# Kernel tuning notes

Hardware: AMD Instinct MI355X
Metric: run time of the kernel (lower is better)

Reference implementation:

```python
import jax, jax.numpy as jnp
import numpy as np

C = 512
GROUPS = 8
EPS = 1e-5


def setup_inputs() -> dict:
    key = jax.random.key(0)
    ks = jax.random.split(key, 7)
    B, H, W = 16, 32, 32
    x = jax.random.normal(ks[0], (B, C, H, W), dtype=jnp.float32)
    gamma = jnp.ones((C,), jnp.float32)
    beta = jnp.zeros((C,), jnp.float32)
    # 1x1 convs stored as [out, in] matrices
    w_qkv = jax.random.normal(ks[1], (3 * C, C), dtype=jnp.float32) * (1.0 / np.sqrt(C))
    b_qkv = jax.random.normal(ks[2], (3 * C,), dtype=jnp.float32) * 0.02
    w_proj = jax.random.normal(ks[3], (C, C), dtype=jnp.float32) * (1.0 / np.sqrt(C))
    b_proj = jax.random.normal(ks[4], (C,), dtype=jnp.float32) * 0.02
    return {"x": x, "gamma": gamma, "beta": beta, "w_qkv": w_qkv,
            "b_qkv": b_qkv, "w_proj": w_proj, "b_proj": b_proj}


def _group_norm(x, gamma, beta):
    B, Cc, H, W = x.shape
    xg = x.reshape(B, GROUPS, Cc // GROUPS, H, W)
    mean = xg.mean(axis=(2, 3, 4), keepdims=True)
    var = xg.var(axis=(2, 3, 4), keepdims=True)
    xg = (xg - mean) * jax.lax.rsqrt(var + EPS)
    x = xg.reshape(B, Cc, H, W)
    return x * gamma[None, :, None, None] + beta[None, :, None, None]


def reference(x, gamma, beta, w_qkv, b_qkv, w_proj, b_proj):
    B, Cc, H, W = x.shape
    N = H * W
    h = _group_norm(x, gamma, beta)  # [B,C,H,W]
    hf = h.reshape(B, Cc, N)  # [B,C,N]
    # 1x1 conv == matmul over channel dim
    qkv = jnp.einsum('oc,bcn->bon', w_qkv, hf) + b_qkv[None, :, None]  # [B,3C,N]
    q, k, v = jnp.split(qkv, 3, axis=1)  # each [B,C,N]
    scale = 1.0 / jnp.sqrt(jnp.float32(Cc))
    # attn[b,i,j] = sum_c q[b,c,i] * k[b,c,j]
    attn = jnp.einsum('bci,bcj->bij', q, k) * scale  # [B,N,N]
    attn = jax.nn.softmax(attn, axis=-1)
    out = jnp.einsum('bij,bcj->bci', attn, v)  # [B,C,N]
    out = jnp.einsum('oc,bcn->bon', w_proj, out) + b_proj[None, :, None]
    return x + out.reshape(B, Cc, H, W)
```

## Files before the change

### kernel.cpp

```cpp
#include <hip/hip_runtime.h>
#include <hip/hip_bf16.h>

typedef unsigned short u16;
typedef unsigned int u32;
typedef __attribute__((ext_vector_type(8))) short short8;
typedef __attribute__((ext_vector_type(4))) float floatx4;

#define BATCH 16
#define CDIM 512
#define NSPAT 1024
#define NGROUP 8

__device__ __forceinline__ u16 f2bf(float f) {
    unsigned u = __float_as_uint(f);
    u += 0x7FFFu + ((u >> 16) & 1u);
    return (u16)(u >> 16);
}
__device__ __forceinline__ u32 f2bf2(float lo, float hi) {
    __hip_bfloat162 h = __float22bfloat162_rn(make_float2(lo, hi));
    return *(u32*)&h;
}

__device__ __forceinline__ void load_lds16(const void* g, void* l) {
    __builtin_amdgcn_global_load_lds(
        (const __attribute__((address_space(1))) unsigned int*)g,
        (__attribute__((address_space(3))) unsigned int*)l, 16, 0, 0);
}

#define SBAR0 __builtin_amdgcn_sched_barrier(0)
#define BARRIER { SBAR0; __builtin_amdgcn_s_barrier(); SBAR0; }

__global__ __launch_bounds__(256) void prep_kernel(
    const float* __restrict__ w_qkv, const float* __restrict__ w_proj,
    const float* __restrict__ b_qkv, const float* __restrict__ x,
    u16* __restrict__ wmega, u16* __restrict__ wproj_bf, u16* __restrict__ wv_t,
    float* __restrict__ stats, float* __restrict__ lsums, float* __restrict__ bpv) {
    int b = blockIdx.x;
    int tid = threadIdx.x;
    if (b < 768) {
        const float* src = (b < 512) ? w_qkv : w_proj;
        u16* dst = (b < 512) ? wmega : wproj_bf;
        int i = (b < 512 ? b : b - 512) * 256 + tid;
        float4 v = ((const float4*)src)[i];
        u32* d = (u32*)dst;
        d[i * 2] = f2bf2(v.x, v.y);
        d[i * 2 + 1] = f2bf2(v.z, v.w);
        return;
    }
    if (b < 832) {
        __shared__ u16 t[64 * 66];
        int bt = b - 768;
        int tx = bt & 7, ty = bt >> 3;
        const float* src = w_qkv + (size_t)(1024 + ty * 64) * CDIM + tx * 64;
#pragma unroll
        for (int p = 0; p < 4; ++p) {
            int r = p * 16 + (tid >> 4);
            int c4 = (tid & 15) << 2;
            float4 v = *(const float4*)(src + (size_t)r * CDIM + c4);
            u16* d = &t[r * 66 + c4];
            d[0] = f2bf(v.x); d[1] = f2bf(v.y); d[2] = f2bf(v.z); d[3] = f2bf(v.w);
        }
        __syncthreads();
        u16* dst = wv_t + (size_t)(tx * 64) * CDIM + ty * 64;
#pragma unroll
        for (int p = 0; p < 4; ++p) {
            int c = p * 16 + (tid >> 4);
            int r4 = (tid & 15) << 2;
            ushort4 o;
            o.x = t[(r4 + 0) * 66 + c];
            o.y = t[(r4 + 1) * 66 + c];
            o.z = t[(r4 + 2) * 66 + c];
            o.w = t[(r4 + 3) * 66 + c];
            *(ushort4*)(dst + (size_t)c * CDIM + r4) = o;
        }
        return;
    }
    if (b < 960) {
        __shared__ float rs[4], rss[4];
        int bg = b - 832;
        const float4* xv = (const float4*)(x + (size_t)bg * 65536);
        float s = 0.f, ss = 0.f;
        for (int i = tid; i < 16384; i += 256) {
            float4 v = xv[i];
            s += v.x + v.y + v.z + v.w;
            ss += v.x * v.x + v.y * v.y + v.z * v.z + v.w * v.w;
        }
#pragma unroll
        for (int off = 32; off; off >>= 1) { s += __shfl_down(s, off); ss += __shfl_down(ss, off); }
        int wave = tid >> 6, lane = tid & 63;
        if (lane == 0) { rs[wave] = s; rss[wave] = ss; }
        __syncthreads();
        if (tid == 0) {
            float S1 = rs[0] + rs[1] + rs[2] + rs[3];
            float S2 = rss[0] + rss[1] + rss[2] + rss[3];
            float mean = S1 * (1.f / 65536.f);
            float var = S2 * (1.f / 65536.f) - mean * mean;
            stats[bg * 2] = mean;
            stats[bg * 2 + 1] = rsqrtf(var + 1e-5f);
        }
        return;
    }
    if (b < 976) {
        ((float4*)lsums)[(b - 960) * 256 + tid] = (float4){0.f, 0.f, 0.f, 0.f};
        return;
    }
    {
        int o0 = (b - 976) * 64;
        int wave = tid >> 6, lane = tid & 63;
        const float4* bvv = (const float4*)(b_qkv + 1024);
        float4 v0 = bvv[lane * 2], v1 = bvv[lane * 2 + 1];
        for (int it = 0; it < 16; ++it) {
            int o = o0 + wave * 16 + it;
            const float4* wr = (const float4*)(w_proj + (size_t)o * CDIM);
            float4 a0 = wr[lane * 2], a1 = wr[lane * 2 + 1];
            float s = a0.x * v0.x + a0.y * v0.y + a0.z * v0.z + a0.w * v0.w
                    + a1.x * v1.x + a1.y * v1.y + a1.z * v1.z + a1.w * v1.w;
#pragma unroll
            for (int off = 32; off; off >>= 1) s += __shfl_down(s, off);
            if (lane == 0) bpv[o] = s;
        }
    }
}

__device__ __forceinline__ void stage_tile(
    const u16* __restrict__ Ab, const u16* __restrict__ Bb, int lda, int ldb,
    int m0, int n0, int k0, u16* As, u16* Bs) {
    int tid = threadIdx.x;
#pragma unroll
    for (int it = 0; it < 4; ++it) {
        int c = it * 256 + tid;
        int r = c >> 3, p = c & 7;
        int kc = p ^ (r & 7);
        load_lds16(Ab + (size_t)(m0 + r) * lda + k0 + (kc << 3), &As[c << 3]);
        load_lds16(Bb + (size_t)(n0 + r) * ldb + k0 + (kc << 3), &Bs[c << 3]);
    }
}

__device__ __forceinline__ void compute_tile(
    const u16* As, const u16* Bs, int wm, int wn, int quad, int lrow,
    floatx4 (&acc)[4][4]) {
#pragma unroll
    for (int s = 0; s < 2; ++s) {
        short8 af[4], bf[4];
#pragma unroll
        for (int i = 0; i < 4; ++i) {
            int R = wm + i * 16 + lrow;
            int p = (s * 4 + quad) ^ (R & 7);
            af[i] = *(const short8*)&As[(R << 6) + (p << 3)];
        }
#pragma unroll
        for (int j = 0; j < 4; ++j) {
            int R = wn + j * 16 + lrow;
            int p = (s * 4 + quad) ^ (R & 7);
            bf[j] = *(const short8*)&Bs[(R << 6) + (p << 3)];
        }
#pragma unroll
        for (int i = 0; i < 4; ++i)
#pragma unroll
            for (int j = 0; j < 4; ++j)
                acc[i][j] = __builtin_amdgcn_mfma_f32_16x16x32_bf16(af[i], bf[j], acc[i][j], 0, 0, 0);
    }
}

__device__ __forceinline__ void gemm_core_sb(
    const u16* __restrict__ Ab, const u16* __restrict__ Bb, int K, int lda, int ldb,
    int m0, int n0, u16* As, u16* Bs, floatx4 (&acc)[4][4]) {
    int tid = threadIdx.x;
    int lane = tid & 63, wave = tid >> 6, quad = lane >> 4, lrow = lane & 15;
    int wm = (wave >> 1) << 6, wn = (wave & 1) << 6;
    for (int k0 = 0; k0 < K; k0 += 64) {
        stage_tile(Ab, Bb, lda, ldb, m0, n0, k0, As, Bs);
        __syncthreads();
        compute_tile(As, Bs, wm, wn, quad, lrow, acc);
        __syncthreads();
    }
}

#define ACC_INIT floatx4 acc[4][4]; \
    _Pragma("unroll") for (int i = 0; i < 4; ++i) \
    _Pragma("unroll") for (int j = 0; j < 4; ++j) acc[i][j] = (floatx4){0.f, 0.f, 0.f, 0.f};

#define EPILOG_IDX int lane = threadIdx.x & 63, wave = threadIdx.x >> 6; \
    int quad = lane >> 4, lrow = lane & 15; \
    int wm = (wave >> 1) << 6, wn = (wave & 1) << 6;

#define ASLOT 16384
#define BSLOT 8192
#define BBASE 49152

__device__ __forceinline__ void issueA3(
    const u16* __restrict__ Ab, int lda, int m0, int t, int slot, u16* smem) {
    int tid = threadIdx.x;
    u16* base = smem + slot * ASLOT;
#pragma unroll
    for (int l = 0; l < 4; ++l) {
        int c = l * 512 + tid;
        int rho = c >> 3, p = c & 7;
        int kc = p ^ (rho & 7);
        load_lds16(Ab + (size_t)(m0 + rho) * lda + (t << 6) + (kc << 3), base + (c << 3));
    }
}
__device__ __forceinline__ void issueB3(
    const u16* __restrict__ Bb, int ldb, int n0, int t, int slot, u16* smem) {
    int tid = threadIdx.x;
    u16* base = smem + BBASE + slot * BSLOT;
#pragma unroll
    for (int l = 0; l < 2; ++l) {
        int c = l * 512 + tid;
        int rho = c >> 3, p = c & 7;
        int kc = p ^ (rho & 7);
        load_lds16(Bb + (size_t)(n0 + rho) * ldb + (t << 6) + (kc << 3), base + (c << 3));
    }
}

__device__ __forceinline__ void gemm256x128_3s(
    const u16* __restrict__ Ab, const u16* __restrict__ Bb, int K, int lda, int ldb,
    int m0, int n0, u16* smem, floatx4 (&acc)[4][4]) {
    int tid = threadIdx.x;
    int lane = tid & 63, wave = tid >> 6;
    int quad = lane >> 4, lrow = lane & 15;
    int wrow = wave >> 1, wcol = wave & 1;
    int nt = K >> 6;
    issueA3(Ab, lda, m0, 0, 0, smem);
    issueB3(Bb, ldb, n0, 0, 0, smem);
    issueA3(Ab, lda, m0, 1, 1, smem);
    issueB3(Bb, ldb, n0, 1, 1, smem);
    int slot = 0, slot2 = 2;
    for (int t = 0; t < nt; ++t) {
        BARRIER;
        if (t + 2 < nt) {
            issueA3(Ab, lda, m0, t + 2, slot2, smem);
            issueB3(Bb, ldb, n0, t + 2, slot2, smem);
            asm volatile("s_waitcnt vmcnt(12)" ::: "memory");
        } else if (t + 1 < nt) {
            asm volatile("s_waitcnt vmcnt(6)" ::: "memory");
        } else {
            asm volatile("s_waitcnt vmcnt(0)" ::: "memory");
        }
        BARRIER;
        const u16* Ah = smem + slot * ASLOT;
        const u16* Bh = smem + BBASE + slot * BSLOT;
        short8 bf[8];
#pragma unroll
        for (int ks = 0; ks < 2; ++ks)
#pragma unroll
            for (int j = 0; j < 4; ++j) {
                int rho = wcol * 64 + j * 16 + lrow;
                int p = (ks * 4 + quad) ^ (lrow & 7);
                bf[ks * 4 + j] = *(const short8*)&Bh[(rho << 6) + (p << 3)];
            }
        short8 af[8];
#pragma unroll
        for (int ks = 0; ks < 2; ++ks)
#pragma unroll
            for (int i = 0; i < 4; ++i) {
                int rho = wrow * 64 + i * 16 + lrow;
                int p = (ks * 4 + quad) ^ (lrow & 7);
                af[ks * 4 + i] = *(const short8*)&Ah[(rho << 6) + (p << 3)];
            }
#pragma unroll
        for (int ks = 0; ks < 2; ++ks)
#pragma unroll
            for (int i = 0; i < 4; ++i)
#pragma unroll
                for (int j = 0; j < 4; ++j)
                    acc[i][j] = __builtin_amdgcn_mfma_f32_16x16x32_bf16(
                        af[ks * 4 + i], bf[ks * 4 + j], acc[i][j], 0, 0, 0);
        slot = (slot == 2) ? 0 : slot + 1;
        slot2 = (slot2 == 2) ? 0 : slot2 + 1;
    }
}

#define ACC_INIT44 floatx4 acc[4][4]; \
    _Pragma("unroll") for (int i = 0; i < 4; ++i) \
    _Pragma("unroll") for (int j = 0; j < 4; ++j) acc[i][j] = (floatx4){0.f, 0.f, 0.f, 0.f};

#define EPILOG_IDX8 int lane = threadIdx.x & 63, wave = threadIdx.x >> 6; \
    int quad = lane >> 4, lrow = lane & 15; \
    int wrow = wave >> 1, wcol = wave & 1;

#define TSTR 66
__global__ __launch_bounds__(256) void gn_wpv_kernel(
    const float* __restrict__ x, const float* __restrict__ gamma, const float* __restrict__ beta,
    const float* __restrict__ stats, u16* __restrict__ hT,
    const u16* __restrict__ wproj_bf, const u16* __restrict__ wv_t, u16* __restrict__ wmega) {
    __shared__ u16 smem[2 * 128 * 64];
    int tid = threadIdx.x;
    if (blockIdx.z == 16) {
        if (blockIdx.x >= 4 || blockIdx.y >= 4) return;
        int m0 = blockIdx.y << 7, n0 = blockIdx.x << 7;
        ACC_INIT;
        gemm_core_sb(wproj_bf, wv_t, CDIM, CDIM, CDIM, m0, n0, smem, smem + 128 * 64, acc);
        EPILOG_IDX;
#pragma unroll
        for (int i = 0; i < 4; ++i)
#pragma unroll
            for (int j = 0; j < 4; ++j)
#pragma unroll
                for (int r = 0; r < 4; ++r) {
                    int R = m0 + wm + i * 16 + (quad << 2) + r;
                    int Cc = n0 + wn + j * 16 + lrow;
                    wmega[(size_t)(1024 + R) * CDIM + Cc] = f2bf(acc[i][j][r]);
                }
        return;
    }
    u16* t = smem;
    int b = blockIdx.z, c0 = blockIdx.y << 6, n0 = blockIdx.x << 6;
    const float* xb = x + ((size_t)b * CDIM + c0) * NSPAT + n0;
#pragma unroll
    for (int p = 0; p < 4; ++p) {
        int cl = p * 16 + (tid >> 4);
        int nl = (tid & 15) << 2;
        int c = c0 + cl;
        int bg = b * NGROUP + (c >> 6);
        float ga = gamma[c] * stats[bg * 2 + 1];
        float be = beta[c] - stats[bg * 2] * ga;
        float4 v = *(const float4*)(xb + (size_t)cl * NSPAT + nl);
        u16* dst = &t[cl * TSTR + nl];
        dst[0] = f2bf(v.x * ga + be);
        dst[1] = f2bf(v.y * ga + be);
        dst[2] = f2bf(v.z * ga + be);
        dst[3] = f2bf(v.w * ga + be);
    }
    __syncthreads();
    u16* hb = hT + ((size_t)b * NSPAT + n0) * CDIM + c0;
#pragma unroll
    for (int p = 0; p < 4; ++p) {
        int nl = p * 16 + (tid >> 4);
        int cl4 = (tid & 15) << 2;
        ushort4 o;
        o.x = t[(cl4 + 0) * TSTR + nl];
        o.y = t[(cl4 + 1) * TSTR + nl];
        o.z = t[(cl4 + 2) * TSTR + nl];
        o.w = t[(cl4 + 3) * TSTR + nl];
        *(ushort4*)(hb + (size_t)nl * CDIM + cl4) = o;
    }
}

__global__ __launch_bounds__(512, 1) void qkv_kernel(
    const u16* __restrict__ wmega, const u16* __restrict__ hT,
    const float* __restrict__ b_qkv, const float* __restrict__ bpv,
    u16* __restrict__ qkT, u16* __restrict__ WV) {
    extern __shared__ u16 smem[];
    int z = blockIdx.x;
    int n0 = blockIdx.y << 7;
    int m0 = blockIdx.z << 8;
    const u16* Bb = hT + (size_t)z * CDIM * NSPAT;
    ACC_INIT44;
    gemm256x128_3s(wmega, Bb, CDIM, CDIM, CDIM, m0, n0, smem, acc);
    EPILOG_IDX8;
    if (blockIdx.z < 4) {
        u16* qk = qkT + (size_t)z * NSPAT * NSPAT;
#pragma unroll
        for (int mf = 0; mf < 4; ++mf) {
            int R0 = m0 + wrow * 64 + mf * 16 + (quad << 2);
            float4 bv = *(const float4*)&b_qkv[R0];
#pragma unroll
            for (int nf = 0; nf < 4; ++nf) {
                int Cc = n0 + wcol * 64 + nf * 16 + lrow;
                uint2 u;
                u.x = f2bf2(acc[mf][nf][0] + bv.x, acc[mf][nf][1] + bv.y);
                u.y = f2bf2(acc[mf][nf][2] + bv.z, acc[mf][nf][3] + bv.w);
                *(uint2*)&qk[(size_t)Cc * NSPAT + R0] = u;
            }
        }
    } else {
        u16* Wp = WV + (size_t)z * CDIM * NSPAT;
#pragma unroll
        for (int mf = 0; mf < 4; ++mf) {
            int R = m0 - 1024 + wrow * 64 + mf * 16 + (quad << 2);
            float4 pv = *(const float4*)&bpv[R];
#pragma unroll
            for (int nf = 0; nf < 4; ++nf) {
                int Cc = n0 + wcol * 64 + nf * 16 + lrow;
                Wp[(size_t)(R + 0) * NSPAT + Cc] = f2bf(acc[mf][nf][0] + pv.x);
                Wp[(size_t)(R + 1) * NSPAT + Cc] = f2bf(acc[mf][nf][1] + pv.y);
                Wp[(size_t)(R + 2) * NSPAT + Cc] = f2bf(acc[mf][nf][2] + pv.z);
                Wp[(size_t)(R + 3) * NSPAT + Cc] = f2bf(acc[mf][nf][3] + pv.w);
            }
        }
    }
}

__global__ __launch_bounds__(512, 1) void scores_kernel(
    const u16* __restrict__ qkT, u16* __restrict__ P, float* __restrict__ lsums, float scale) {
    extern __shared__ u16 smem[];
    int z = blockIdx.x;
    int n0 = blockIdx.y << 7;
    int m0 = blockIdx.z << 8;
    const u16* qb = qkT + (size_t)z * NSPAT * NSPAT;
    ACC_INIT44;
    gemm256x128_3s(qb + CDIM, qb, CDIM, NSPAT, NSPAT, m0, n0, smem, acc);
    EPILOG_IDX8;
    u16* Pp = P + (size_t)z * NSPAT * NSPAT;
    float* ls = lsums + (size_t)z * NSPAT;
#pragma unroll
    for (int nf = 0; nf < 4; ++nf) {
        int Ci = n0 + wcol * 64 + nf * 16 + lrow;
        float part = 0.f;
#pragma unroll
        for (int mf = 0; mf < 4; ++mf) {
            int Rj0 = m0 + wrow * 64 + mf * 16 + (quad << 2);
            float e0 = __expf(acc[mf][nf][0] * scale);
            float e1 = __expf(acc[mf][nf][1] * scale);
            float e2 = __expf(acc[mf][nf][2] * scale);
            float e3 = __expf(acc[mf][nf][3] * scale);
            part += (e0 + e1) + (e2 + e3);
            uint2 u;
            u.x = f2bf2(e0, e1);
            u.y = f2bf2(e2, e3);
            *(uint2*)&Pp[(size_t)Ci * NSPAT + Rj0] = u;
        }
        part += __shfl_xor(part, 16);
        part += __shfl_xor(part, 32);
        if (lane < 16) atomicAdd(&ls[Ci], part);
    }
}

__global__ __launch_bounds__(512, 1) void final_kernel(
    const u16* __restrict__ WV, const u16* __restrict__ P, const float* __restrict__ lsums,
    const float* __restrict__ bias, const float* __restrict__ x, float* __restrict__ out) {
    extern __shared__ u16 smem[];
    int z = blockIdx.x;
    int n0 = blockIdx.y << 7;
    int m0 = blockIdx.z << 8;
    const u16* Pb = P + (size_t)z * NSPAT * NSPAT;
    const u16* WVb = WV + (size_t)z * CDIM * NSPAT;
    ACC_INIT44;
    gemm256x128_3s(Pb, WVb, NSPAT, NSPAT, NSPAT, m0, n0, smem, acc);
    EPILOG_IDX8;
    float* Op = out + (size_t)z * CDIM * NSPAT;
    const float* xr = x + (size_t)z * CDIM * NSPAT;
    const float* li = lsums + (size_t)z * NSPAT;
#pragma unroll
    for (int mf = 0; mf < 4; ++mf) {
        int Ri0 = m0 + wrow * 64 + mf * 16 + (quad << 2);
        float4 lv = *(const float4*)&li[Ri0];
        float s0 = __builtin_amdgcn_rcpf(lv.x);
        float s1 = __builtin_amdgcn_rcpf(lv.y);
        float s2 = __builtin_amdgcn_rcpf(lv.z);
        float s3 = __builtin_amdgcn_rcpf(lv.w);
#pragma unroll
        for (int nf = 0; nf < 4; ++nf) {
            int Co = n0 + wcol * 64 + nf * 16 + lrow;
            float bv = bias[Co];
            size_t off = (size_t)Co * NSPAT + Ri0;
            float4 xv = *(const float4*)&xr[off];
            float4 o;
            o.x = acc[mf][nf][0] * s0 + bv + xv.x;
            o.y = acc[mf][nf][1] * s1 + bv + xv.y;
            o.z = acc[mf][nf][2] * s2 + bv + xv.z;
            o.w = acc[mf][nf][3] * s3 + bv + xv.w;
            *(float4*)&Op[off] = o;
        }
    }
}

extern "C" void kernel_launch(void* const* d_in, const int* in_sizes, int n_in,
                              void* d_out, int out_size, void* d_ws, size_t ws_size,
                              hipStream_t stream) {
    const float* x      = (const float*)d_in[0];
    const float* gamma  = (const float*)d_in[1];
    const float* beta   = (const float*)d_in[2];
    const float* w_qkv  = (const float*)d_in[3];
    const float* b_qkv  = (const float*)d_in[4];
    const float* w_proj = (const float*)d_in[5];
    const float* b_proj = (const float*)d_in[6];
    float* out = (float*)d_out;

    const size_t CN = (size_t)CDIM * NSPAT;
    const size_t NN = (size_t)NSPAT * NSPAT;
    const float SCALE = 0.044194173824159216f;
    const int LDS_3S = (3 * (ASLOT + BSLOT)) * 2;

    static bool lds_attr_done = false;
    if (!lds_attr_done) {
        hipFuncSetAttribute((const void*)qkv_kernel,
                            hipFuncAttributeMaxDynamicSharedMemorySize, LDS_3S);
        hipFuncSetAttribute((const void*)scores_kernel,
                            hipFuncAttributeMaxDynamicSharedMemorySize, LDS_3S);
        hipFuncSetAttribute((const void*)final_kernel,
                            hipFuncAttributeMaxDynamicSharedMemorySize, LDS_3S);
        lds_attr_done = true;
    }

    char* ws = (char*)d_ws;
    float* stats   = (float*)ws;
    float* bpv     = (float*)(ws + 1024);
    u16* wmega     = (u16*)(ws + 4096);
    u16* wproj_bf  = wmega + (size_t)3 * CDIM * CDIM;
    u16* wv_t      = wproj_bf + (size_t)CDIM * CDIM;
    u16* hT        = wv_t + (size_t)CDIM * CDIM;
    u16* qkT       = hT + BATCH * CN;
    u16* WV        = qkT + BATCH * NN;
    u16* P         = WV + BATCH * CN;
    float* lsums   = (float*)(P + BATCH * NN);

    prep_kernel<<<984, 256, 0, stream>>>(
        w_qkv, w_proj, b_qkv, x, wmega, wproj_bf, wv_t, stats, lsums, bpv);

    gn_wpv_kernel<<<dim3(16, 8, 17), 256, 0, stream>>>(
        x, gamma, beta, stats, hT, wproj_bf, wv_t, wmega);

    qkv_kernel<<<dim3(BATCH, 8, 6), 512, LDS_3S, stream>>>(
        wmega, hT, b_qkv, bpv, qkT, WV);

    scores_kernel<<<dim3(BATCH, 8, 4), 512, LDS_3S, stream>>>(qkT, P, lsums, SCALE);

    final_kernel<<<dim3(BATCH, 4, 4), 512, LDS_3S, stream>>>(WV, P, lsums, b_proj, x, out);
}
```

Before: 140.9 us.

## Loop multiple M-tiles per block and reorder grid so batch is slowest

The qkv and scores kernels now have each workgroup compute several 256-row tiles in a loop (3 for qkv, 2 for scores), so they launch 256 blocks instead of 768 or 512. A leading barrier is added to the GEMM so LDS can be safely reused between iterations. All three GEMM kernels reorder the grid so the batch index is blockIdx.z, which groups tiles of the same batch together for L2 reuse of the shared operand. The intent is to cut block scheduling tail effects and improve cache locality on a 256-CU device. The cost is longer serial work per block with no overlap between consecutive tiles.

```diff
diff --git a/kernel.cpp b/kernel.cpp
--- a/kernel.cpp
+++ b/kernel.cpp
@@ -221,6 +221,7 @@
     int quad = lane >> 4, lrow = lane & 15;
     int wrow = wave >> 1, wcol = wave & 1;
     int nt = K >> 6;
+    BARRIER;
     issueA3(Ab, lda, m0, 0, 0, smem);
     issueB3(Bb, ldb, n0, 0, 0, smem);
     issueA3(Ab, lda, m0, 1, 1, smem);
@@ -342,41 +343,45 @@
     const float* __restrict__ b_qkv, const float* __restrict__ bpv,
     u16* __restrict__ qkT, u16* __restrict__ WV) {
     extern __shared__ u16 smem[];
-    int z = blockIdx.x;
+    int z = blockIdx.z;
     int n0 = blockIdx.y << 7;
-    int m0 = blockIdx.z << 8;
     const u16* Bb = hT + (size_t)z * CDIM * NSPAT;
-    ACC_INIT44;
-    gemm256x128_3s(wmega, Bb, CDIM, CDIM, CDIM, m0, n0, smem, acc);
     EPILOG_IDX8;
-    if (blockIdx.z < 4) {
-        u16* qk = qkT + (size_t)z * NSPAT * NSPAT;
-#pragma unroll
-        for (int mf = 0; mf < 4; ++mf) {
-            int R0 = m0 + wrow * 64 + mf * 16 + (quad << 2);
-            float4 bv = *(const float4*)&b_qkv[R0];
-#pragma unroll
-            for (int nf = 0; nf < 4; ++nf) {
-                int Cc = n0 + wcol * 64 + nf * 16 + lrow;
-                uint2 u;
-                u.x = f2bf2(acc[mf][nf][0] + bv.x, acc[mf][nf][1] + bv.y);
-                u.y = f2bf2(acc[mf][nf][2] + bv.z, acc[mf][nf][3] + bv.w);
-                *(uint2*)&qk[(size_t)Cc * NSPAT + R0] = u;
+    u16* qk = qkT + (size_t)z * NSPAT * NSPAT;
+    u16* Wp = WV + (size_t)z * CDIM * NSPAT;
+#pragma unroll 1
+    for (int mi = 0; mi < 3; ++mi) {
+        int mt = blockIdx.x * 3 + mi;
+        int m0 = mt << 8;
+        ACC_INIT44;
+        gemm256x128_3s(wmega, Bb, CDIM, CDIM, CDIM, m0, n0, smem, acc);
+        if (mt < 4) {
+#pragma unroll
+            for (int mf = 0; mf < 4; ++mf) {
+                int R0 = m0 + wrow * 64 + mf * 16 + (quad << 2);
+                float4 bv = *(const float4*)&b_qkv[R0];
+#pragma unroll
+                for (int nf = 0; nf < 4; ++nf) {
+                    int Cc = n0 + wcol * 64 + nf * 16 + lrow;
+                    uint2 u;
+                    u.x = f2bf2(acc[mf][nf][0] + bv.x, acc[mf][nf][1] + bv.y);
+                    u.y = f2bf2(acc[mf][nf][2] + bv.z, acc[mf][nf][3] + bv.w);
+                    *(uint2*)&qk[(size_t)Cc * NSPAT + R0] = u;
+                }
             }
-        }
-    } else {
-        u16* Wp = WV + (size_t)z * CDIM * NSPAT;
-#pragma unroll
-        for (int mf = 0; mf < 4; ++mf) {
-            int R = m0 - 1024 + wrow * 64 + mf * 16 + (quad << 2);
-            float4 pv = *(const float4*)&bpv[R];
-#pragma unroll
-            for (int nf = 0; nf < 4; ++nf) {
-                int Cc = n0 + wcol * 64 + nf * 16 + lrow;
-                Wp[(size_t)(R + 0) * NSPAT + Cc] = f2bf(acc[mf][nf][0] + pv.x);
-                Wp[(size_t)(R + 1) * NSPAT + Cc] = f2bf(acc[mf][nf][1] + pv.y);
-                Wp[(size_t)(R + 2) * NSPAT + Cc] = f2bf(acc[mf][nf][2] + pv.z);
-                Wp[(size_t)(R + 3) * NSPAT + Cc] = f2bf(acc[mf][nf][3] + pv.w);
+        } else {
+#pragma unroll
+            for (int mf = 0; mf < 4; ++mf) {
+                int R = m0 - 1024 + wrow * 64 + mf * 16 + (quad << 2);
+                float4 pv = *(const float4*)&bpv[R];
+#pragma unroll
+                for (int nf = 0; nf < 4; ++nf) {
+                    int Cc = n0 + wcol * 64 + nf * 16 + lrow;
+                    Wp[(size_t)(R + 0) * NSPAT + Cc] = f2bf(acc[mf][nf][0] + pv.x);
+                    Wp[(size_t)(R + 1) * NSPAT + Cc] = f2bf(acc[mf][nf][1] + pv.y);
+                    Wp[(size_t)(R + 2) * NSPAT + Cc] = f2bf(acc[mf][nf][2] + pv.z);
+                    Wp[(size_t)(R + 3) * NSPAT + Cc] = f2bf(acc[mf][nf][3] + pv.w);
+                }
             }
         }
     }
@@ -385,35 +390,38 @@
 __global__ __launch_bounds__(512, 1) void scores_kernel(
     const u16* __restrict__ qkT, u16* __restrict__ P, float* __restrict__ lsums, float scale) {
     extern __shared__ u16 smem[];
-    int z = blockIdx.x;
+    int z = blockIdx.z;
     int n0 = blockIdx.y << 7;
-    int m0 = blockIdx.z << 8;
     const u16* qb = qkT + (size_t)z * NSPAT * NSPAT;
-    ACC_INIT44;
-    gemm256x128_3s(qb + CDIM, qb, CDIM, NSPAT, NSPAT, m0, n0, smem, acc);
     EPILOG_IDX8;
     u16* Pp = P + (size_t)z * NSPAT * NSPAT;
     float* ls = lsums + (size_t)z * NSPAT;
-#pragma unroll
-    for (int nf = 0; nf < 4; ++nf) {
-        int Ci = n0 + wcol * 64 + nf * 16 + lrow;
-        float part = 0.f;
-#pragma unroll
-        for (int mf = 0; mf < 4; ++mf) {
-            int Rj0 = m0 + wrow * 64 + mf * 16 + (quad << 2);
-            float e0 = __expf(acc[mf][nf][0] * scale);
-            float e1 = __expf(acc[mf][nf][1] * scale);
-            float e2 = __expf(acc[mf][nf][2] * scale);
-            float e3 = __expf(acc[mf][nf][3] * scale);
-            part += (e0 + e1) + (e2 + e3);
-            uint2 u;
-            u.x = f2bf2(e0, e1);
-            u.y = f2bf2(e2, e3);
-            *(uint2*)&Pp[(size_t)Ci * NSPAT + Rj0] = u;
-        }
-        part += __shfl_xor(part, 16);
-        part += __shfl_xor(part, 32);
-        if (lane < 16) atomicAdd(&ls[Ci], part);
+#pragma unroll 1
+    for (int ji = 0; ji < 2; ++ji) {
+        int m0 = (blockIdx.x * 2 + ji) << 8;
+        ACC_INIT44;
+        gemm256x128_3s(qb + CDIM, qb, CDIM, NSPAT, NSPAT, m0, n0, smem, acc);
+#pragma unroll
+        for (int nf = 0; nf < 4; ++nf) {
+            int Ci = n0 + wcol * 64 + nf * 16 + lrow;
+            float part = 0.f;
+#pragma unroll
+            for (int mf = 0; mf < 4; ++mf) {
+                int Rj0 = m0 + wrow * 64 + mf * 16 + (quad << 2);
+                float e0 = __expf(acc[mf][nf][0] * scale);
+                float e1 = __expf(acc[mf][nf][1] * scale);
+                float e2 = __expf(acc[mf][nf][2] * scale);
+                float e3 = __expf(acc[mf][nf][3] * scale);
+                part += (e0 + e1) + (e2 + e3);
+                uint2 u;
+                u.x = f2bf2(e0, e1);
+                u.y = f2bf2(e2, e3);
+                *(uint2*)&Pp[(size_t)Ci * NSPAT + Rj0] = u;
+            }
+            part += __shfl_xor(part, 16);
+            part += __shfl_xor(part, 32);
+            if (lane < 16) atomicAdd(&ls[Ci], part);
+        }
     }
 }
 
@@ -421,9 +429,9 @@
     const u16* __restrict__ WV, const u16* __restrict__ P, const float* __restrict__ lsums,
     const float* __restrict__ bias, const float* __restrict__ x, float* __restrict__ out) {
     extern __shared__ u16 smem[];
-    int z = blockIdx.x;
-    int n0 = blockIdx.y << 7;
-    int m0 = blockIdx.z << 8;
+    int z = blockIdx.z;
+    int n0 = blockIdx.x << 7;
+    int m0 = blockIdx.y << 8;
     const u16* Pb = P + (size_t)z * NSPAT * NSPAT;
     const u16* WVb = WV + (size_t)z * CDIM * NSPAT;
     ACC_INIT44;
@@ -502,10 +510,10 @@
     gn_wpv_kernel<<<dim3(16, 8, 17), 256, 0, stream>>>(
         x, gamma, beta, stats, hT, wproj_bf, wv_t, wmega);
 
-    qkv_kernel<<<dim3(BATCH, 8, 6), 512, LDS_3S, stream>>>(
+    qkv_kernel<<<dim3(2, 8, BATCH), 512, LDS_3S, stream>>>(
         wmega, hT, b_qkv, bpv, qkT, WV);
 
-    scores_kernel<<<dim3(BATCH, 8, 4), 512, LDS_3S, stream>>>(qkT, P, lsums, SCALE);
-
-    final_kernel<<<dim3(BATCH, 4, 4), 512, LDS_3S, stream>>>(WV, P, lsums, b_proj, x, out);
-}
+    scores_kernel<<<dim3(2, 8, BATCH), 512, LDS_3S, stream>>>(qkT, P, lsums, SCALE);
+
+    final_kernel<<<dim3(4, 4, BATCH), 512, LDS_3S, stream>>>(WV, P, lsums, b_proj, x, out);
+}
```

After: 151.2 us. 7.3% more time.
